# Performance work log

Hardware: AMD Instinct MI355X
Metric: run time of the kernel (lower is better)

## Reference

```python
import jax, jax.numpy as jnp
import numpy as np

B, S, HID = 1, 2048, 2880
H, KV, D = 64, 8, 64
WINDOW = 128
SCALE = D ** -0.5
NEG_INF = jnp.float32(-1e30)


def _rope_cos_sin():
    # realistic RoPE tables over full head_dim (HF rotate_half convention)
    inv_freq = 1.0 / (10000.0 ** (np.arange(0, D, 2, dtype=np.float32) / D))
    t = np.arange(S, dtype=np.float32)
    freqs = np.outer(t, inv_freq)                      # [S, D/2]
    emb = np.concatenate([freqs, freqs], axis=-1)      # [S, D]
    return jnp.asarray(np.cos(emb))[None], jnp.asarray(np.sin(emb))[None]


def setup_inputs() -> dict:
    key = jax.random.key(0)
    ks = jax.random.split(key, 10)
    cos, sin = _rope_cos_sin()
    sd = lambda fan_in: 1.0 / np.sqrt(fan_in)
    return {
        "hidden_states": jax.random.normal(ks[0], (B, S, HID), jnp.float32),
        "cos": cos, "sin": sin,
        "Wq": jax.random.normal(ks[1], (HID, H * D), jnp.float32) * sd(HID),
        "bq": jax.random.normal(ks[2], (H * D,), jnp.float32) * 0.02,
        "Wk": jax.random.normal(ks[3], (HID, KV * D), jnp.float32) * sd(HID),
        "bk": jax.random.normal(ks[4], (KV * D,), jnp.float32) * 0.02,
        "Wv": jax.random.normal(ks[5], (HID, KV * D), jnp.float32) * sd(HID),
        "bv": jax.random.normal(ks[6], (KV * D,), jnp.float32) * 0.02,
        "Wo": jax.random.normal(ks[7], (H * D, HID), jnp.float32) * sd(H * D),
        "bo": jax.random.normal(ks[8], (HID,), jnp.float32) * 0.02,
        "sinks": jax.random.normal(ks[9], (H,), jnp.float32),
    }


def _rotate_half(x):
    x1, x2 = jnp.split(x, 2, axis=-1)
    return jnp.concatenate([-x2, x1], axis=-1)


def _forward(hidden_states, cos, sin, Wq, bq, Wk, bk, Wv, bv, Wo, bo, sinks):
    q = (hidden_states @ Wq + bq).reshape(B, S, H, D)
    k = (hidden_states @ Wk + bk).reshape(B, S, KV, D)
    v = (hidden_states @ Wv + bv).reshape(B, S, KV, D)
    # RoPE with explicit cos/sin, unsqueeze at head dim (bsnd layout)
    c, s = cos[:, :, None, :], sin[:, :, None, :]
    q = q * c + _rotate_half(q) * s
    k = k * c + _rotate_half(k) * s
    # GQA: expand kv heads to match query heads
    k = jnp.repeat(k, H // KV, axis=2)
    v = jnp.repeat(v, H // KV, axis=2)
    scores = jnp.einsum("bqhd,bkhd->bhqk", q, k) * SCALE  # [B,H,S,S]
    i = jnp.arange(S)[:, None]
    j = jnp.arange(S)[None, :]
    allowed = (j <= i) & (j > i - WINDOW)                  # causal + sliding window
    scores = jnp.where(allowed, scores, NEG_INF)
    # sink-augmented softmax: sinks act as an extra logit per head, dropped after norm
    m = jnp.maximum(scores.max(axis=-1), sinks[None, :, None])  # [B,H,S]
    p = jnp.exp(scores - m[..., None])                      # [B,H,S,S]
    denom = p.sum(axis=-1) + jnp.exp(sinks[None, :, None] - m)  # [B,H,S]
    attn = jnp.einsum("bhqk,bkhd->bqhd", p, v) / denom.transpose(0, 2, 1)[..., None]
    return attn.reshape(B, S, H * D) @ Wo + bo


def reference(hidden_states, cos, sin, Wq, bq, Wk, bk, Wv, bv, Wo, bo, sinks):
    return _forward(hidden_states, cos, sin, Wq, bq, Wk, bk, Wv, bv, Wo, bo, sinks)
```

## Files before the change

### kernel.cpp

```cpp
#include <hip/hip_runtime.h>

typedef unsigned short u16;
typedef __bf16 bf16x8 __attribute__((ext_vector_type(8)));
typedef float f32x4 __attribute__((ext_vector_type(4)));

constexpr int SEQ = 2048;
constexpr int HIDN = 2880;
constexpr int NQKV = 5120;
constexpr float SCALE = 0.125f;
constexpr float NEG_INF = -1e30f;

#define ASM_VMCNT(n)  asm volatile("s_waitcnt vmcnt(" #n ")" ::: "memory")
#define ASM_LGKM(n)   asm volatile("s_waitcnt lgkmcnt(" #n ")" ::: "memory")
#define ASM_BARRIER() asm volatile("s_barrier" ::: "memory")
#define SCHEDBAR()    __builtin_amdgcn_sched_barrier(0)

__device__ __forceinline__ u16 f2bf(float f) {
  unsigned int u = __builtin_bit_cast(unsigned int, f);
  u += 0x7FFFu + ((u >> 16) & 1u);
  return (u16)(u >> 16);
}
__device__ __forceinline__ float bf2f(u16 h) {
  unsigned int u = ((unsigned int)h) << 16;
  return __builtin_bit_cast(float, u);
}
__device__ __forceinline__ void async_load16(const void* g, void* l) {
  __builtin_amdgcn_global_load_lds(
      (const __attribute__((address_space(1))) unsigned int*)g,
      (__attribute__((address_space(3))) unsigned int*)l, 16, 0, 0);
}
__device__ __forceinline__ f32x4 DSR(unsigned addr) {
  f32x4 d;
  asm volatile("ds_read_b128 %0, %1" : "=v"(d) : "v"(addr));
  return d;
}
__device__ __forceinline__ bf16x8 asbf(f32x4 v) { return __builtin_bit_cast(bf16x8, v); }

__global__ __launch_bounds__(256) void conv_f2b(const float* __restrict__ in,
                                                u16* __restrict__ out, long n4) {
  long i = (long)blockIdx.x * 256 + threadIdx.x;
  if (i >= n4) return;
  float4 v = ((const float4*)in)[i];
  u16 o0 = f2bf(v.x), o1 = f2bf(v.y), o2 = f2bf(v.z), o3 = f2bf(v.w);
  out[i * 4 + 0] = o0; out[i * 4 + 1] = o1; out[i * 4 + 2] = o2; out[i * 4 + 3] = o3;
}

__global__ __launch_bounds__(256) void transpose_f2b(const float* __restrict__ in,
                                                     u16* __restrict__ out,
                                                     int R, int C, int ostride) {
  __shared__ float tile[32][33];
  int c0 = blockIdx.x * 32, r0 = blockIdx.y * 32;
  int tx = threadIdx.x & 31, ty = threadIdx.x >> 5;
#pragma unroll
  for (int i = 0; i < 32; i += 8)
    tile[ty + i][tx] = in[(long)(r0 + ty + i) * C + c0 + tx];
  __syncthreads();
#pragma unroll
  for (int i = 0; i < 32; i += 8)
    out[(long)(c0 + ty + i) * ostride + r0 + tx] = f2bf(tile[tx][ty + i]);
}

__global__ __launch_bounds__(256) void concat_bias(const float* bq, const float* bk,
                                                   const float* bv, float* out) {
  int t = blockIdx.x * 256 + threadIdx.x;
  if (t < 4096) out[t] = bq[t];
  else if (t < 4608) out[t] = bk[t - 4096];
  else if (t < 5120) out[t] = bv[t - 4608];
}

template <bool OUT_BF16>
__global__ __launch_bounds__(256, 2) void gemm_kb(const u16* __restrict__ A,
                                                  const u16* __restrict__ B,
                                                  const float* __restrict__ bias,
                                                  void* __restrict__ Cout,
                                                  int N, int K) {
  __shared__ u16 lds[3 * 12288];
  const int tid = threadIdx.x, lane = tid & 63, wn = tid >> 6;
  const int lr = lane & 15, lk = lane >> 4;

  const int gm = gridDim.x;
  int nwg = gm * gridDim.y;
  int bid = blockIdx.y * gm + blockIdx.x;
  int q8 = nwg >> 3, r8 = nwg & 7;
  int xcd = bid & 7, seq = bid >> 3;
  int swz = (xcd < r8 ? xcd * (q8 + 1) : r8 * (q8 + 1) + (xcd - r8) * q8) + seq;
  const long brow = (long)(swz % gm) * 128;
  const long bcol = (long)(swz / gm) * 256;
  const int nkt = K >> 5;

  const int ca0 = tid, ca1 = tid + 256;
  const u16* As0 = A + (brow + (ca0 >> 2)) * (long)K + ((ca0 & 3) ^ ((ca0 >> 3) & 3)) * 8;
  const u16* As1 = A + (brow + (ca1 >> 2)) * (long)K + ((ca1 & 3) ^ ((ca1 >> 3) & 3)) * 8;
  const u16* Bsr[4];
#pragma unroll
  for (int i = 0; i < 4; ++i) {
    int c = tid + 256 * i;
    Bsr[i] = B + (bcol + (c >> 2)) * (long)K + ((c & 3) ^ ((c >> 3) & 3)) * 8;
  }
  char* L = (char*)lds;
  auto stage = [&](int kt, int b) {
    long ko = (long)kt * 32;
    char* d = L + b * 24576;
    async_load16(As0 + ko, d + ca0 * 16);
    async_load16(As1 + ko, d + ca1 * 16);
#pragma unroll
    for (int i = 0; i < 4; ++i)
      async_load16(Bsr[i] + ko, d + 8192 + (tid + 256 * i) * 16);
  };

  const unsigned lds0 = (unsigned)(size_t)L;
  const unsigned xs = (unsigned)((lk ^ ((lr >> 1) & 3)) << 4);
  const unsigned aoff = lds0 + (unsigned)(lr * 64) + xs;
  const unsigned boff = lds0 + 8192u + (unsigned)((wn * 64 + lr) * 64) + xs;

  f32x4 acc[8][4] = {};
  stage(0, 0);
  if (nkt > 1) stage(1, 1);

  int b = 0, sb = 2;
  for (int t = 0; t < nkt; ++t) {
    if (t + 2 < nkt)      { stage(t + 2, sb); ASM_VMCNT(12); }
    else if (t + 1 < nkt) { ASM_VMCNT(6); }
    else                  { ASM_VMCNT(0); }
    ASM_BARRIER();

    const unsigned ab = aoff + (unsigned)(b * 24576);
    const unsigned bb = boff + (unsigned)(b * 24576);
    f32x4 af[8], bf4[4];
#pragma unroll
    for (int m = 0; m < 4; ++m) af[m] = DSR(ab + m * 1024u);
#pragma unroll
    for (int n = 0; n < 4; ++n) bf4[n] = DSR(bb + n * 1024u);
#pragma unroll
    for (int m = 4; m < 8; ++m) af[m] = DSR(ab + m * 1024u);
    ASM_LGKM(4); SCHEDBAR();
    __builtin_amdgcn_s_setprio(1);
#pragma unroll
    for (int m = 0; m < 4; ++m)
#pragma unroll
      for (int n = 0; n < 4; ++n)
        acc[m][n] = __builtin_amdgcn_mfma_f32_16x16x32_bf16(asbf(af[m]), asbf(bf4[n]), acc[m][n], 0, 0, 0);
    __builtin_amdgcn_s_setprio(0);
    ASM_LGKM(0); SCHEDBAR();
    __builtin_amdgcn_s_setprio(1);
#pragma unroll
    for (int m = 4; m < 8; ++m)
#pragma unroll
      for (int n = 0; n < 4; ++n)
        acc[m][n] = __builtin_amdgcn_mfma_f32_16x16x32_bf16(asbf(af[m]), asbf(bf4[n]), acc[m][n], 0, 0, 0);
    __builtin_amdgcn_s_setprio(0);
    ASM_BARRIER();
    b = (b == 2) ? 0 : b + 1;
    sb = (sb == 2) ? 0 : sb + 1;
  }

#pragma unroll
  for (int m = 0; m < 8; ++m) {
    long row = brow + m * 16 + lk * 4;
#pragma unroll
    for (int n = 0; n < 4; ++n) {
      long col = bcol + wn * 64 + n * 16 + lr;
      if (col < N) {
        float bv = bias[col];
#pragma unroll
        for (int r = 0; r < 4; ++r) {
          float v = acc[m][n][r] + bv;
          if (OUT_BF16) ((u16*)Cout)[(row + r) * (long)N + col] = f2bf(v);
          else          ((float*)Cout)[(row + r) * (long)N + col] = v;
        }
      }
    }
  }
}

__global__ __launch_bounds__(256) void rope_kernel(u16* __restrict__ QKV,
                                                   const float* __restrict__ cosb,
                                                   const float* __restrict__ sinb) {
  long idx = (long)blockIdx.x * 256 + threadIdx.x;
  if (idx >= (long)SEQ * 72 * 32) return;
  int d = idx & 31;
  int h = (int)((idx >> 5) % 72);
  int s = (int)(idx / (72 * 32));
  int col = (h < 64) ? h * 64 : 4096 + (h - 64) * 64;
  u16* p = QKV + (long)s * NQKV + col;
  float x1 = bf2f(p[d]), x2 = bf2f(p[d + 32]);
  float c = cosb[s * 64 + d], sn = sinb[s * 64 + d];
  p[d]      = f2bf(x1 * c - x2 * sn);
  p[d + 32] = f2bf(x2 * c + x1 * sn);
}

__global__ __launch_bounds__(256, 1) void attn_kernel(const u16* __restrict__ QKV,
                                                      const float* __restrict__ sinks,
                                                      u16* __restrict__ Oa) {
  __shared__ u16 Ks[64 * 64];
  __shared__ u16 Vt[64 * 64];
  __shared__ u16 Ps[4][64 * 72];
  const int tid = threadIdx.x, wid = tid >> 6, lane = tid & 63;
  const int lr = lane & 15, lk = lane >> 4;
  const int i0 = blockIdx.x * 64;
  const int h = blockIdx.y * 4 + wid;
  const int g = h >> 3;

  bf16x8 qf[4][2];
#pragma unroll
  for (int m = 0; m < 4; ++m)
#pragma unroll
    for (int kc = 0; kc < 2; ++kc)
      qf[m][kc] = *(const bf16x8*)&QKV[(long)(i0 + m * 16 + lr) * NQKV + h * 64 + kc * 32 + lk * 8];

  const float sinkh = sinks[h];
  float mrun[4][4], lrun[4][4];
  f32x4 oacc[4][4] = {};
#pragma unroll
  for (int m = 0; m < 4; ++m)
#pragma unroll
    for (int r = 0; r < 4; ++r) { mrun[m][r] = sinkh; lrun[m][r] = 0.f; }

  const int jb0 = (i0 >= 128) ? (i0 - 128) : 0;
  for (int jb = jb0; jb <= i0; jb += 64) {
#pragma unroll
    for (int i = 0; i < 2; ++i) {
      int c = wid * 128 + i * 64 + lane;
      int row = c >> 3, sp = c & 7;
      int ssrc = sp ^ (row & 7);
      async_load16(QKV + (long)(jb + row) * NQKV + 4096 + g * 64 + ssrc * 8,
                   ((char*)Ks) + c * 16);
    }
    {
      int j0 = (tid & 31) * 2, d0 = (tid >> 5) * 8;
      const u16* vp = QKV + (long)(jb + j0) * NQKV + 4608 + g * 64 + d0;
      int4 rv0 = *(const int4*)vp;
      int4 rv1 = *(const int4*)(vp + NQKV);
      const u16* a0 = (const u16*)&rv0;
      const u16* a1 = (const u16*)&rv1;
#pragma unroll
      for (int e = 0; e < 8; ++e) {
        int d = d0 + e;
        unsigned val = (unsigned)a0[e] | ((unsigned)a1[e] << 16);
        int byt = d * 128 + ((((j0 >> 3) ^ (d & 7)) << 4)) + ((j0 & 7) * 2);
        *(unsigned*)((char*)Vt + byt) = val;
      }
    }
    __syncthreads();

    f32x4 sf[4][4] = {};
    __builtin_amdgcn_s_setprio(1);
#pragma unroll
    for (int kc = 0; kc < 2; ++kc) {
      bf16x8 kf[4];
#pragma unroll
      for (int cf = 0; cf < 4; ++cf) {
        int row = cf * 16 + lr;
        kf[cf] = *(const bf16x8*)((const char*)Ks + row * 128 + (((kc * 4 + lk) ^ (lr & 7)) << 4));
      }
#pragma unroll
      for (int m = 0; m < 4; ++m)
#pragma unroll
        for (int cf = 0; cf < 4; ++cf)
          sf[m][cf] = __builtin_amdgcn_mfma_f32_16x16x32_bf16(qf[m][kc], kf[cf], sf[m][cf], 0, 0, 0);
    }
    __builtin_amdgcn_s_setprio(0);

#pragma unroll
    for (int m = 0; m < 4; ++m) {
      float rmax[4];
#pragma unroll
      for (int r = 0; r < 4; ++r) {
        int i = i0 + m * 16 + lk * 4 + r;
        float mx = NEG_INF;
#pragma unroll
        for (int cf = 0; cf < 4; ++cf) {
          int j = jb + cf * 16 + lr;
          float v = sf[m][cf][r] * SCALE;
          bool ok = (j <= i) && (j > i - 128);
          v = ok ? v : NEG_INF;
          sf[m][cf][r] = v;
          mx = fmaxf(mx, v);
        }
#pragma unroll
        for (int off = 1; off < 16; off <<= 1) mx = fmaxf(mx, __shfl_xor(mx, off, 64));
        rmax[r] = mx;
      }
#pragma unroll
      for (int r = 0; r < 4; ++r) {
        float mnew = fmaxf(mrun[m][r], rmax[r]);
        float corr = __expf(mrun[m][r] - mnew);
        mrun[m][r] = mnew;
        float rsum = 0.f;
#pragma unroll
        for (int cf = 0; cf < 4; ++cf) {
          float p = __expf(sf[m][cf][r] - mnew);
          sf[m][cf][r] = p;
          rsum += p;
        }
#pragma unroll
        for (int off = 1; off < 16; off <<= 1) rsum += __shfl_xor(rsum, off, 64);
        lrun[m][r] = lrun[m][r] * corr + rsum;
#pragma unroll
        for (int dn = 0; dn < 4; ++dn) oacc[m][dn][r] *= corr;
      }
    }

#pragma unroll
    for (int m = 0; m < 4; ++m)
#pragma unroll
      for (int cf = 0; cf < 4; ++cf)
#pragma unroll
        for (int r = 0; r < 4; ++r)
          Ps[wid][(m * 16 + lk * 4 + r) * 72 + cf * 16 + lr] = f2bf(sf[m][cf][r]);
    __syncthreads();

    __builtin_amdgcn_s_setprio(1);
#pragma unroll
    for (int kc = 0; kc < 2; ++kc) {
      bf16x8 pf[4], vf[4];
#pragma unroll
      for (int m = 0; m < 4; ++m)
        pf[m] = *(const bf16x8*)&Ps[wid][(m * 16 + lr) * 72 + kc * 32 + lk * 8];
#pragma unroll
      for (int dn = 0; dn < 4; ++dn) {
        int row = dn * 16 + lr;
        vf[dn] = *(const bf16x8*)((const char*)Vt + row * 128 + (((kc * 4 + lk) ^ (lr & 7)) << 4));
      }
#pragma unroll
      for (int m = 0; m < 4; ++m)
#pragma unroll
        for (int dn = 0; dn < 4; ++dn)
          oacc[m][dn] = __builtin_amdgcn_mfma_f32_16x16x32_bf16(pf[m], vf[dn], oacc[m][dn], 0, 0, 0);
    }
    __builtin_amdgcn_s_setprio(0);
    __syncthreads();
  }

#pragma unroll
  for (int m = 0; m < 4; ++m)
#pragma unroll
    for (int r = 0; r < 4; ++r) {
      float denom = lrun[m][r] + __expf(sinkh - mrun[m][r]);
      float inv = 1.f / denom;
      long row = i0 + m * 16 + lk * 4 + r;
#pragma unroll
      for (int dn = 0; dn < 4; ++dn)
        Oa[row * 4096 + h * 64 + dn * 16 + lr] = f2bf(oacc[m][dn][r] * inv);
    }
}

extern "C" void kernel_launch(void* const* d_in, const int* in_sizes, int n_in,
                              void* d_out, int out_size, void* d_ws, size_t ws_size,
                              hipStream_t stream) {
  const float* X    = (const float*)d_in[0];
  const float* cosb = (const float*)d_in[1];
  const float* sinb = (const float*)d_in[2];
  const float* Wq   = (const float*)d_in[3];
  const float* bq   = (const float*)d_in[4];
  const float* Wk   = (const float*)d_in[5];
  const float* bk   = (const float*)d_in[6];
  const float* Wv   = (const float*)d_in[7];
  const float* bv   = (const float*)d_in[8];
  const float* Wo   = (const float*)d_in[9];
  const float* bo   = (const float*)d_in[10];
  const float* sinks = (const float*)d_in[11];

  char* ws = (char*)d_ws;
  size_t off = 0;
  auto alloc = [&](size_t bytes) -> void* {
    void* p = ws + off;
    off += (bytes + 255) & ~(size_t)255;
    return p;
  };
  u16*   Xb    = (u16*)alloc((size_t)SEQ * HIDN * 2);
  u16*   Wqkv  = (u16*)alloc((size_t)NQKV * HIDN * 2);
  u16*   Wot   = (u16*)alloc((size_t)3072 * 4096 * 2);
  float* bqkv  = (float*)alloc((size_t)NQKV * 4);
  u16*   QKV   = (u16*)alloc((size_t)SEQ * NQKV * 2);
  u16*   Ab    = (u16*)alloc((size_t)SEQ * 4096 * 2);
  (void)ws_size; (void)in_sizes; (void)n_in; (void)out_size;

  conv_f2b<<<(SEQ * HIDN / 4 + 255) / 256, 256, 0, stream>>>(X, Xb, (long)SEQ * HIDN / 4);
  transpose_f2b<<<dim3(4096 / 32, HIDN / 32), 256, 0, stream>>>(Wq, Wqkv, HIDN, 4096, HIDN);
  transpose_f2b<<<dim3(512 / 32, HIDN / 32), 256, 0, stream>>>(Wk, Wqkv + (size_t)4096 * HIDN, HIDN, 512, HIDN);
  transpose_f2b<<<dim3(512 / 32, HIDN / 32), 256, 0, stream>>>(Wv, Wqkv + (size_t)4608 * HIDN, HIDN, 512, HIDN);
  transpose_f2b<<<dim3(HIDN / 32, 4096 / 32), 256, 0, stream>>>(Wo, Wot, 4096, HIDN, 4096);
  concat_bias<<<(NQKV + 255) / 256, 256, 0, stream>>>(bq, bk, bv, bqkv);
  gemm_kb<true><<<dim3(SEQ / 128, NQKV / 256), 256, 0, stream>>>(Xb, Wqkv, bqkv, QKV, NQKV, HIDN);
  rope_kernel<<<(int)(((long)SEQ * 72 * 32 + 255) / 256), 256, 0, stream>>>(QKV, cosb, sinb);
  attn_kernel<<<dim3(SEQ / 64, 64 / 4), 256, 0, stream>>>(QKV, sinks, Ab);
  gemm_kb<false><<<dim3(SEQ / 128, 3072 / 256), 256, 0, stream>>>(Ab, Wot, bo, (float*)d_out, HIDN, 4096);
}
```

Baseline: 262.7 us.

## Split GEMM tile across eight waves with double-buffered LDS

The 128x256 GEMM tile is now computed by 512 threads (8 waves in a 2x4 grid) instead of 4 waves. Each wave holds a 64x64 accumulator instead of 128x64, which halves accumulator registers. The LDS pipeline drops from triple to double buffering, freeing LDS so more waves can be resident. The aim is more latency hiding through higher occupancy, at the cost of shallower prefetch and more barrier participants per block.

Result: faster. 253.1 us (-3.6%).

```diff
diff --git a/kernel.cpp b/kernel.cpp
--- a/kernel.cpp
+++ b/kernel.cpp
@@ -69,13 +69,14 @@
 }
 
 template <bool OUT_BF16>
-__global__ __launch_bounds__(256, 2) void gemm_kb(const u16* __restrict__ A,
+__global__ __launch_bounds__(512, 4) void gemm_w8(const u16* __restrict__ A,
                                                   const u16* __restrict__ B,
                                                   const float* __restrict__ bias,
                                                   void* __restrict__ Cout,
                                                   int N, int K) {
-  __shared__ u16 lds[3 * 12288];
-  const int tid = threadIdx.x, lane = tid & 63, wn = tid >> 6;
+  __shared__ u16 lds[2 * 12288];
+  const int tid = threadIdx.x, lane = tid & 63, wid = tid >> 6;
+  const int wm = wid >> 2, wn = wid & 3;
   const int lr = lane & 15, lk = lane >> 4;
 
   const int gm = gridDim.x;
@@ -88,75 +89,54 @@
   const long bcol = (long)(swz / gm) * 256;
   const int nkt = K >> 5;
 
-  const int ca0 = tid, ca1 = tid + 256;
-  const u16* As0 = A + (brow + (ca0 >> 2)) * (long)K + ((ca0 & 3) ^ ((ca0 >> 3) & 3)) * 8;
-  const u16* As1 = A + (brow + (ca1 >> 2)) * (long)K + ((ca1 & 3) ^ ((ca1 >> 3) & 3)) * 8;
-  const u16* Bsr[4];
-#pragma unroll
-  for (int i = 0; i < 4; ++i) {
-    int c = tid + 256 * i;
-    Bsr[i] = B + (bcol + (c >> 2)) * (long)K + ((c & 3) ^ ((c >> 3) & 3)) * 8;
-  }
+  const int c1 = tid + 512;
+  const u16* As0 = A + (brow + (tid >> 2)) * (long)K + ((tid & 3) ^ ((tid >> 3) & 3)) * 8;
+  const u16* Bs0 = B + (bcol + (tid >> 2)) * (long)K + ((tid & 3) ^ ((tid >> 3) & 3)) * 8;
+  const u16* Bs1 = B + (bcol + (c1 >> 2)) * (long)K + ((c1 & 3) ^ ((c1 >> 3) & 3)) * 8;
   char* L = (char*)lds;
   auto stage = [&](int kt, int b) {
     long ko = (long)kt * 32;
     char* d = L + b * 24576;
-    async_load16(As0 + ko, d + ca0 * 16);
-    async_load16(As1 + ko, d + ca1 * 16);
-#pragma unroll
-    for (int i = 0; i < 4; ++i)
-      async_load16(Bsr[i] + ko, d + 8192 + (tid + 256 * i) * 16);
+    async_load16(As0 + ko, d + tid * 16);
+    async_load16(Bs0 + ko, d + 8192 + tid * 16);
+    async_load16(Bs1 + ko, d + 8192 + c1 * 16);
   };
 
   const unsigned lds0 = (unsigned)(size_t)L;
   const unsigned xs = (unsigned)((lk ^ ((lr >> 1) & 3)) << 4);
-  const unsigned aoff = lds0 + (unsigned)(lr * 64) + xs;
+  const unsigned aoff = lds0 + (unsigned)((wm * 64 + lr) * 64) + xs;
   const unsigned boff = lds0 + 8192u + (unsigned)((wn * 64 + lr) * 64) + xs;
 
-  f32x4 acc[8][4] = {};
+  f32x4 acc[4][4] = {};
   stage(0, 0);
-  if (nkt > 1) stage(1, 1);
-
-  int b = 0, sb = 2;
+
   for (int t = 0; t < nkt; ++t) {
-    if (t + 2 < nkt)      { stage(t + 2, sb); ASM_VMCNT(12); }
-    else if (t + 1 < nkt) { ASM_VMCNT(6); }
-    else                  { ASM_VMCNT(0); }
+    const int b = t & 1;
+    if (t + 1 < nkt) { stage(t + 1, b ^ 1); ASM_VMCNT(3); }
+    else             { ASM_VMCNT(0); }
     ASM_BARRIER();
 
     const unsigned ab = aoff + (unsigned)(b * 24576);
     const unsigned bb = boff + (unsigned)(b * 24576);
-    f32x4 af[8], bf4[4];
+    f32x4 af[4], bf4[4];
 #pragma unroll
     for (int m = 0; m < 4; ++m) af[m] = DSR(ab + m * 1024u);
 #pragma unroll
     for (int n = 0; n < 4; ++n) bf4[n] = DSR(bb + n * 1024u);
-#pragma unroll
-    for (int m = 4; m < 8; ++m) af[m] = DSR(ab + m * 1024u);
-    ASM_LGKM(4); SCHEDBAR();
-    __builtin_amdgcn_s_setprio(1);
-#pragma unroll
-    for (int m = 0; m < 4; ++m)
-#pragma unroll
-      for (int n = 0; n < 4; ++n)
-        acc[m][n] = __builtin_amdgcn_mfma_f32_16x16x32_bf16(asbf(af[m]), asbf(bf4[n]), acc[m][n], 0, 0, 0);
-    __builtin_amdgcn_s_setprio(0);
     ASM_LGKM(0); SCHEDBAR();
     __builtin_amdgcn_s_setprio(1);
 #pragma unroll
-    for (int m = 4; m < 8; ++m)
+    for (int m = 0; m < 4; ++m)
 #pragma unroll
       for (int n = 0; n < 4; ++n)
         acc[m][n] = __builtin_amdgcn_mfma_f32_16x16x32_bf16(asbf(af[m]), asbf(bf4[n]), acc[m][n], 0, 0, 0);
     __builtin_amdgcn_s_setprio(0);
     ASM_BARRIER();
-    b = (b == 2) ? 0 : b + 1;
-    sb = (sb == 2) ? 0 : sb + 1;
   }
 
 #pragma unroll
-  for (int m = 0; m < 8; ++m) {
-    long row = brow + m * 16 + lk * 4;
+  for (int m = 0; m < 4; ++m) {
+    long row = brow + wm * 64 + m * 16 + lk * 4;
 #pragma unroll
     for (int n = 0; n < 4; ++n) {
       long col = bcol + wn * 64 + n * 16 + lr;
@@ -382,8 +362,8 @@
   transpose_f2b<<<dim3(512 / 32, HIDN / 32), 256, 0, stream>>>(Wv, Wqkv + (size_t)4608 * HIDN, HIDN, 512, HIDN);
   transpose_f2b<<<dim3(HIDN / 32, 4096 / 32), 256, 0, stream>>>(Wo, Wot, 4096, HIDN, 4096);
   concat_bias<<<(NQKV + 255) / 256, 256, 0, stream>>>(bq, bk, bv, bqkv);
-  gemm_kb<true><<<dim3(SEQ / 128, NQKV / 256), 256, 0, stream>>>(Xb, Wqkv, bqkv, QKV, NQKV, HIDN);
+  gemm_w8<true><<<dim3(SEQ / 128, NQKV / 256), 512, 0, stream>>>(Xb, Wqkv, bqkv, QKV, NQKV, HIDN);
   rope_kernel<<<(int)(((long)SEQ * 72 * 32 + 255) / 256), 256, 0, stream>>>(QKV, cosb, sinb);
   attn_kernel<<<dim3(SEQ / 64, 64 / 4), 256, 0, stream>>>(QKV, sinks, Ab);
-  gemm_kb<false><<<dim3(SEQ / 128, 3072 / 256), 256, 0, stream>>>(Ab, Wot, bo, (float*)d_out, HIDN, 4096);
-}
+  gemm_w8<false><<<dim3(SEQ / 128, 3072 / 256), 512, 0, stream>>>(Ab, Wot, bo, (float*)d_out, HIDN, 4096);
+}
```

## Fuse RoPE into QKV GEMM epilogue, split-K output GEMM, restage LDS pipeline

Applied to the files above, without the earlier changes.

Rewrites the GEMM main loop so A tiles are triple-buffered and B tiles double-buffered, with loads interleaved between the two MFMA halves and a smaller LDS footprint. RoPE moves into the QKV GEMM epilogue, which removes a separate read-modify-write pass over Q and K. The output projection uses split-K across two z-slices to raise the block count from 192 to 384, and a combine kernel then sums the partials and adds the bias. The cost is an extra fp32 partial buffer (reusing the Wqkv workspace) and an extra elementwise pass.

Result: faster. 246.8 us (-6.0%).

```diff
diff --git a/kernel.cpp b/kernel.cpp
--- a/kernel.cpp
+++ b/kernel.cpp
@@ -68,14 +68,17 @@
   else if (t < 5120) out[t] = bv[t - 4608];
 }
 
-template <bool OUT_BF16>
-__global__ __launch_bounds__(256, 2) void gemm_kb(const u16* __restrict__ A,
-                                                  const u16* __restrict__ B,
+template <int MODE>
+__global__ __launch_bounds__(256, 2) void gemm_p2(const u16* __restrict__ A,
+                                                  const u16* __restrict__ Bp,
                                                   const float* __restrict__ bias,
-                                                  void* __restrict__ Cout,
-                                                  int N, int K) {
-  __shared__ u16 lds[3 * 12288];
-  const int tid = threadIdx.x, lane = tid & 63, wn = tid >> 6;
+                                                  const float* __restrict__ cosb,
+                                                  const float* __restrict__ sinb,
+                                                  void* __restrict__ out0,
+                                                  float* __restrict__ out1,
+                                                  int N, int Kst, int nkt) {
+  __shared__ u16 lds[28672];
+  const int tid = threadIdx.x, lane = tid & 63, wid = tid >> 6;
   const int lr = lane & 15, lk = lane >> 4;
 
   const int gm = gridDim.x;
@@ -86,107 +89,143 @@
   int swz = (xcd < r8 ? xcd * (q8 + 1) : r8 * (q8 + 1) + (xcd - r8) * q8) + seq;
   const long brow = (long)(swz % gm) * 128;
   const long bcol = (long)(swz / gm) * 256;
-  const int nkt = K >> 5;
-
-  const int ca0 = tid, ca1 = tid + 256;
-  const u16* As0 = A + (brow + (ca0 >> 2)) * (long)K + ((ca0 & 3) ^ ((ca0 >> 3) & 3)) * 8;
-  const u16* As1 = A + (brow + (ca1 >> 2)) * (long)K + ((ca1 & 3) ^ ((ca1 >> 3) & 3)) * 8;
-  const u16* Bsr[4];
+  const long kbase = (MODE == 1) ? (long)blockIdx.z * nkt * 32 : 0;
+
+  char* L = (char*)lds;
+  const u16* Asrc[2];
+  const u16* Bsrc[4];
+#pragma unroll
+  for (int i = 0; i < 2; ++i) {
+    int c = tid + 256 * i;
+    Asrc[i] = A + (brow + (c >> 2)) * (long)Kst + kbase + ((c & 3) ^ ((c >> 3) & 3)) * 8;
+  }
 #pragma unroll
   for (int i = 0; i < 4; ++i) {
     int c = tid + 256 * i;
-    Bsr[i] = B + (bcol + (c >> 2)) * (long)K + ((c & 3) ^ ((c >> 3) & 3)) * 8;
+    Bsrc[i] = Bp + (bcol + (c >> 2)) * (long)Kst + kbase + ((c & 3) ^ ((c >> 3) & 3)) * 8;
   }
-  char* L = (char*)lds;
-  auto stage = [&](int kt, int b) {
-    long ko = (long)kt * 32;
-    char* d = L + b * 24576;
-    async_load16(As0 + ko, d + ca0 * 16);
-    async_load16(As1 + ko, d + ca1 * 16);
+  auto stageA = [&](int kt, int ab) {
+    char* d = L + ab * 8192;
+    async_load16(Asrc[0] + (long)kt * 32, d + tid * 16);
+    async_load16(Asrc[1] + (long)kt * 32, d + (tid + 256) * 16);
+  };
+  auto stageB = [&](int kt) {
+    char* d = L + 24576 + (kt & 1) * 16384;
 #pragma unroll
     for (int i = 0; i < 4; ++i)
-      async_load16(Bsr[i] + ko, d + 8192 + (tid + 256 * i) * 16);
+      async_load16(Bsrc[i] + (long)kt * 32, d + (tid + 256 * i) * 16);
   };
 
   const unsigned lds0 = (unsigned)(size_t)L;
   const unsigned xs = (unsigned)((lk ^ ((lr >> 1) & 3)) << 4);
   const unsigned aoff = lds0 + (unsigned)(lr * 64) + xs;
-  const unsigned boff = lds0 + 8192u + (unsigned)((wn * 64 + lr) * 64) + xs;
+  const unsigned boff = lds0 + 24576u + (unsigned)((wid * 64 + lr) * 64) + xs;
 
   f32x4 acc[8][4] = {};
-  stage(0, 0);
-  if (nkt > 1) stage(1, 1);
-
-  int b = 0, sb = 2;
+  stageA(0, 0); stageB(0); stageA(1, 1); stageB(1);
+  ASM_VMCNT(6);
+  ASM_BARRIER();
+
+  int a3 = 0;
   for (int t = 0; t < nkt; ++t) {
-    if (t + 2 < nkt)      { stage(t + 2, sb); ASM_VMCNT(12); }
-    else if (t + 1 < nkt) { ASM_VMCNT(6); }
-    else                  { ASM_VMCNT(0); }
+    const unsigned ab = aoff + (unsigned)(a3 * 8192);
+    const unsigned bb = boff + (unsigned)((t & 1) * 16384);
+    const bool s2 = (t + 2 < nkt);
+    const int a3n = (a3 == 2) ? 0 : a3 + 1;
+    const int a3s = (a3n == 2) ? 0 : a3n + 1;
+    f32x4 a[4], b[4];
+#pragma unroll
+    for (int mf = 0; mf < 4; ++mf) a[mf] = DSR(ab + mf * 1024u);
+#pragma unroll
+    for (int nf = 0; nf < 4; ++nf) b[nf] = DSR(bb + nf * 1024u);
+    if (s2) stageA(t + 2, a3s);
     ASM_BARRIER();
-
-    const unsigned ab = aoff + (unsigned)(b * 24576);
-    const unsigned bb = boff + (unsigned)(b * 24576);
-    f32x4 af[8], bf4[4];
-#pragma unroll
-    for (int m = 0; m < 4; ++m) af[m] = DSR(ab + m * 1024u);
-#pragma unroll
-    for (int n = 0; n < 4; ++n) bf4[n] = DSR(bb + n * 1024u);
-#pragma unroll
-    for (int m = 4; m < 8; ++m) af[m] = DSR(ab + m * 1024u);
-    ASM_LGKM(4); SCHEDBAR();
-    __builtin_amdgcn_s_setprio(1);
-#pragma unroll
-    for (int m = 0; m < 4; ++m)
-#pragma unroll
-      for (int n = 0; n < 4; ++n)
-        acc[m][n] = __builtin_amdgcn_mfma_f32_16x16x32_bf16(asbf(af[m]), asbf(bf4[n]), acc[m][n], 0, 0, 0);
-    __builtin_amdgcn_s_setprio(0);
     ASM_LGKM(0); SCHEDBAR();
     __builtin_amdgcn_s_setprio(1);
 #pragma unroll
-    for (int m = 4; m < 8; ++m)
-#pragma unroll
-      for (int n = 0; n < 4; ++n)
-        acc[m][n] = __builtin_amdgcn_mfma_f32_16x16x32_bf16(asbf(af[m]), asbf(bf4[n]), acc[m][n], 0, 0, 0);
+    for (int mf = 0; mf < 4; ++mf)
+#pragma unroll
+      for (int nf = 0; nf < 4; ++nf)
+        acc[mf][nf] = __builtin_amdgcn_mfma_f32_16x16x32_bf16(asbf(a[mf]), asbf(b[nf]), acc[mf][nf], 0, 0, 0);
     __builtin_amdgcn_s_setprio(0);
     ASM_BARRIER();
-    b = (b == 2) ? 0 : b + 1;
-    sb = (sb == 2) ? 0 : sb + 1;
+#pragma unroll
+    for (int mf = 0; mf < 4; ++mf) a[mf] = DSR(ab + (mf + 4) * 1024u);
+    if (s2) stageB(t + 2);
+    ASM_BARRIER();
+    ASM_LGKM(0); SCHEDBAR();
+    __builtin_amdgcn_s_setprio(1);
+#pragma unroll
+    for (int mf = 0; mf < 4; ++mf)
+#pragma unroll
+      for (int nf = 0; nf < 4; ++nf)
+        acc[mf + 4][nf] = __builtin_amdgcn_mfma_f32_16x16x32_bf16(asbf(a[mf]), asbf(b[nf]), acc[mf + 4][nf], 0, 0, 0);
+    __builtin_amdgcn_s_setprio(0);
+    if (s2) { ASM_VMCNT(6); } else { ASM_VMCNT(0); }
+    ASM_BARRIER();
+    a3 = a3n;
   }
 
-#pragma unroll
-  for (int m = 0; m < 8; ++m) {
-    long row = brow + m * 16 + lk * 4;
-#pragma unroll
-    for (int n = 0; n < 4; ++n) {
-      long col = bcol + wn * 64 + n * 16 + lr;
-      if (col < N) {
-        float bv = bias[col];
-#pragma unroll
-        for (int r = 0; r < 4; ++r) {
-          float v = acc[m][n][r] + bv;
-          if (OUT_BF16) ((u16*)Cout)[(row + r) * (long)N + col] = f2bf(v);
-          else          ((float*)Cout)[(row + r) * (long)N + col] = v;
+  const int col0 = (int)bcol + wid * 64;
+  if (MODE == 0) {
+    const bool rope = (col0 < 4608);
+#pragma unroll
+    for (int mf = 0; mf < 8; ++mf) {
+      long row = brow + mf * 16 + lk * 4;
+#pragma unroll
+      for (int r = 0; r < 4; ++r) {
+        long s = row + r;
+        if (rope) {
+#pragma unroll
+          for (int nf = 0; nf < 2; ++nf) {
+            int col = col0 + nf * 16 + lr;
+            int d = nf * 16 + lr;
+            float c = cosb[s * 64 + d], sn = sinb[s * 64 + d];
+            float x1 = acc[mf][nf][r] + bias[col];
+            float x2 = acc[mf][nf + 2][r] + bias[col + 32];
+            ((u16*)out0)[s * (long)N + col]      = f2bf(x1 * c - x2 * sn);
+            ((u16*)out0)[s * (long)N + col + 32] = f2bf(x2 * c + x1 * sn);
+          }
+        } else {
+#pragma unroll
+          for (int nf = 0; nf < 4; ++nf) {
+            int col = col0 + nf * 16 + lr;
+            ((u16*)out0)[s * (long)N + col] = f2bf(acc[mf][nf][r] + bias[col]);
+          }
         }
       }
     }
+  } else {
+    float* o = (blockIdx.z == 0) ? (float*)out0 : out1;
+#pragma unroll
+    for (int mf = 0; mf < 8; ++mf) {
+      long row = brow + mf * 16 + lk * 4;
+#pragma unroll
+      for (int nf = 0; nf < 4; ++nf) {
+        int col = col0 + nf * 16 + lr;
+        if (col < N) {
+#pragma unroll
+          for (int r = 0; r < 4; ++r)
+            o[(row + r) * (long)N + col] = acc[mf][nf][r];
+        }
+      }
+    }
   }
 }
 
-__global__ __launch_bounds__(256) void rope_kernel(u16* __restrict__ QKV,
-                                                   const float* __restrict__ cosb,
-                                                   const float* __restrict__ sinb) {
-  long idx = (long)blockIdx.x * 256 + threadIdx.x;
-  if (idx >= (long)SEQ * 72 * 32) return;
-  int d = idx & 31;
-  int h = (int)((idx >> 5) % 72);
-  int s = (int)(idx / (72 * 32));
-  int col = (h < 64) ? h * 64 : 4096 + (h - 64) * 64;
-  u16* p = QKV + (long)s * NQKV + col;
-  float x1 = bf2f(p[d]), x2 = bf2f(p[d + 32]);
-  float c = cosb[s * 64 + d], sn = sinb[s * 64 + d];
-  p[d]      = f2bf(x1 * c - x2 * sn);
-  p[d + 32] = f2bf(x2 * c + x1 * sn);
+__global__ __launch_bounds__(256) void combine_out(const float* __restrict__ P1,
+                                                   const float* __restrict__ bias,
+                                                   float* __restrict__ out) {
+  long i = (long)blockIdx.x * 256 + threadIdx.x;
+  if (i >= (long)SEQ * HIDN / 4) return;
+  int c4 = (int)(i % (HIDN / 4));
+  float4 p0 = ((const float4*)out)[i];
+  float4 p1 = ((const float4*)P1)[i];
+  float4 b = ((const float4*)bias)[c4];
+  float4 r;
+  r.x = p0.x + p1.x + b.x; r.y = p0.y + p1.y + b.y;
+  r.z = p0.z + p1.z + b.z; r.w = p0.w + p1.w + b.w;
+  ((float4*)out)[i] = r;
 }
 
 __global__ __launch_bounds__(256, 1) void attn_kernel(const u16* __restrict__ QKV,
@@ -374,6 +413,7 @@
   float* bqkv  = (float*)alloc((size_t)NQKV * 4);
   u16*   QKV   = (u16*)alloc((size_t)SEQ * NQKV * 2);
   u16*   Ab    = (u16*)alloc((size_t)SEQ * 4096 * 2);
+  float* Pt1 = (float*)Wqkv;
   (void)ws_size; (void)in_sizes; (void)n_in; (void)out_size;
 
   conv_f2b<<<(SEQ * HIDN / 4 + 255) / 256, 256, 0, stream>>>(X, Xb, (long)SEQ * HIDN / 4);
@@ -382,8 +422,10 @@
   transpose_f2b<<<dim3(512 / 32, HIDN / 32), 256, 0, stream>>>(Wv, Wqkv + (size_t)4608 * HIDN, HIDN, 512, HIDN);
   transpose_f2b<<<dim3(HIDN / 32, 4096 / 32), 256, 0, stream>>>(Wo, Wot, 4096, HIDN, 4096);
   concat_bias<<<(NQKV + 255) / 256, 256, 0, stream>>>(bq, bk, bv, bqkv);
-  gemm_kb<true><<<dim3(SEQ / 128, NQKV / 256), 256, 0, stream>>>(Xb, Wqkv, bqkv, QKV, NQKV, HIDN);
-  rope_kernel<<<(int)(((long)SEQ * 72 * 32 + 255) / 256), 256, 0, stream>>>(QKV, cosb, sinb);
+  gemm_p2<0><<<dim3(16, 20, 1), 256, 0, stream>>>(Xb, Wqkv, bqkv, cosb, sinb,
+                                                  QKV, nullptr, NQKV, HIDN, 90);
   attn_kernel<<<dim3(SEQ / 64, 64 / 4), 256, 0, stream>>>(QKV, sinks, Ab);
-  gemm_kb<false><<<dim3(SEQ / 128, 3072 / 256), 256, 0, stream>>>(Ab, Wot, bo, (float*)d_out, HIDN, 4096);
-}
+  gemm_p2<1><<<dim3(16, 12, 2), 256, 0, stream>>>(Ab, Wot, nullptr, nullptr, nullptr,
+                                                  d_out, Pt1, HIDN, 4096, 64);
+  combine_out<<<(SEQ * HIDN / 4 + 255) / 256, 256, 0, stream>>>(Pt1, bo, (float*)d_out);
+}
```
